# Performance work log

Measured on AMD Instinct MI355X. Metric: run time of the kernel, lower is better.

Reference implementation:

```python
import jax, jax.numpy as jnp
import numpy as np

D_IN = 1024
D_OUT = 1024
NUM_HEADS = 16
HEAD_DIM = D_OUT // NUM_HEADS


def setup_inputs() -> dict:
    key = jax.random.key(0)
    k_x, k_q, k_k, k_v, k_o = jax.random.split(key, 5)
    # Xavier-uniform-ish init for weights (stored as [d_in, d_out] for x @ W)
    lim = float(np.sqrt(6.0 / (D_IN + D_OUT)) / np.sqrt(2.0))
    lim_o = float(np.sqrt(6.0 / (D_OUT + D_OUT)))
    return {
        "x": jax.random.normal(k_x, (2, 2048, D_IN), dtype=jnp.float32),
        "W_query": jax.random.uniform(k_q, (D_IN, D_OUT), jnp.float32, -lim, lim),
        "W_key": jax.random.uniform(k_k, (D_IN, D_OUT), jnp.float32, -lim, lim),
        "W_value": jax.random.uniform(k_v, (D_IN, D_OUT), jnp.float32, -lim, lim),
        "W_out": jax.random.uniform(k_o, (D_OUT, D_OUT), jnp.float32, -lim_o, lim_o),
        "b_out": jnp.zeros((D_OUT,), dtype=jnp.float32),
    }


def reference(x, W_query, W_key, W_value, W_out, b_out):
    B, S, _ = x.shape
    scale = 1.0 / np.sqrt(HEAD_DIM)

    def split_heads(t):  # [B,S,D] -> [B,H,S,hd]
        return t.reshape(B, S, NUM_HEADS, HEAD_DIM).transpose(0, 2, 1, 3)

    q = split_heads(x @ W_query)
    k = split_heads(x @ W_key)
    v = split_heads(x @ W_value)

    scores = jnp.einsum("bhqd,bhkd->bhqk", q, k) * scale  # [B,H,S,S]
    causal = jnp.tril(jnp.ones((S, S), dtype=bool))  # True = keep
    scores = jnp.where(causal, scores, -jnp.inf)
    weights = jax.nn.softmax(scores, axis=-1)
    ctx = jnp.einsum("bhqk,bhkd->bhqd", weights, v)
    ctx = ctx.transpose(0, 2, 1, 3).reshape(B, S, D_OUT)
    return ctx @ W_out + b_out
```

## Files before the change

kernel.cpp:

```cpp
#include <hip/hip_runtime.h>
#include <hip/hip_bf16.h>


typedef __bf16 bf16_t;
typedef __bf16 bf16x4 __attribute__((ext_vector_type(4)));
typedef __bf16 bf16x8 __attribute__((ext_vector_type(8)));
typedef float f32x4 __attribute__((ext_vector_type(4)));

__device__ __forceinline__ void barrier_lgkm() {
    asm volatile("s_waitcnt lgkmcnt(0)\n\ts_barrier" ::: "memory");
}

__device__ __forceinline__ float exp_pwrite(f32x4 sc[4], bf16_t* Ps,
                                            int wave, int quad, int l16) {
    float part = 0.f;
    int rowbase = (wave * 16 + l16) * 64;
    int gran = (quad & 1) * 4;
    int chi = quad >> 1;
#pragma unroll
    for (int nt = 0; nt < 4; nt++) {
        f32x4 p;
#pragma unroll
        for (int rr = 0; rr < 4; rr++) {
            p[rr] = __builtin_amdgcn_exp2f(sc[nt][rr]);
            part += p[rr];
        }
        bf16x4 pb;
#pragma unroll
        for (int rr = 0; rr < 4; rr++) pb[rr] = (bf16_t)p[rr];
        int cc = (nt * 2 + chi) ^ (l16 & 7);
        *(bf16x4*)(Ps + rowbase + cc * 8 + gran) = pb;
    }
    part += __shfl_xor(part, 16);
    part += __shfl_xor(part, 32);
    return part;
}

__global__ __launch_bounds__(256) void prep_k(
    const float* __restrict__ x, const float* __restrict__ W0,
    const float* __restrict__ W1, const float* __restrict__ W2,
    const float* __restrict__ W3, bf16_t* __restrict__ xb,
    bf16_t* __restrict__ WTs) {
    __shared__ bf16_t T[64][65];
    int t = threadIdx.x;
    int blk = blockIdx.x;
    if (blk < 4096) {
        int i = blk * 256 + t;
        float4 v = ((const float4*)x)[i];
        bf16x4 o;
        o[0] = (bf16_t)v.x; o[1] = (bf16_t)v.y;
        o[2] = (bf16_t)v.z; o[3] = (bf16_t)v.w;
        ((bf16x4*)xb)[i] = o;
        return;
    }
    int jj = blk - 4096;
    int k0 = (jj & 15) * 64, n0 = ((jj >> 4) & 15) * 64, z = jj >> 8;
    const float* W = (z == 0) ? W0 : (z == 1) ? W1 : (z == 2) ? W2 : W3;
    bf16_t* WT = WTs + (size_t)z * 1048576;
#pragma unroll
    for (int c = 0; c < 4; c++) {
        int idx = c * 256 + t;
        int row = idx >> 4, col4 = (idx & 15) * 4;
        float4 v = *(const float4*)(W + (k0 + row) * 1024 + n0 + col4);
        T[row][col4 + 0] = (bf16_t)v.x;
        T[row][col4 + 1] = (bf16_t)v.y;
        T[row][col4 + 2] = (bf16_t)v.z;
        T[row][col4 + 3] = (bf16_t)v.w;
    }
    __syncthreads();
#pragma unroll
    for (int c = 0; c < 4; c++) {
        int idx = c * 256 + t;
        int nrow = idx >> 4, kc4 = (idx & 15) * 4;
        bf16x4 o;
        o[0] = T[kc4 + 0][nrow];
        o[1] = T[kc4 + 1][nrow];
        o[2] = T[kc4 + 2][nrow];
        o[3] = T[kc4 + 3][nrow];
        *(bf16x4*)(WT + (n0 + nrow) * 1024 + k0 + kc4) = o;
    }
}

__global__ __launch_bounds__(256) void qkv_k(
    const bf16_t* __restrict__ xb, const bf16_t* __restrict__ WTs,
    bf16_t* __restrict__ Qb, bf16_t* __restrict__ Kb, bf16_t* __restrict__ Vb) {
    const int KD = 1024;
    __shared__ __align__(16) bf16_t As[2][4096];
    __shared__ __align__(16) bf16_t Bs[2][4096];
    int tid = threadIdx.x;
    int wave = tid >> 6, lane = tid & 63;
    int quad = lane >> 4, l16 = lane & 15;
    int wm = wave >> 1, wn = wave & 1;
    int z = blockIdx.z;
    const bf16_t* BT = WTs + (size_t)z * 1048576;
    int m0 = blockIdx.x * 128;
    int n0 = blockIdx.y * 128;

    int r = tid >> 2;
    int c8 = (((tid & 3) ^ ((tid >> 3) & 3))) * 8;
    const bf16_t* gA0 = xb + (size_t)(m0 + r) * KD + c8;
    const bf16_t* gA1 = xb + (size_t)(m0 + 64 + r) * KD + c8;
    const bf16_t* gB0 = BT + (size_t)(n0 + r) * KD + c8;
    const bf16_t* gB1 = BT + (size_t)(n0 + 64 + r) * KD + c8;

    f32x4 acc[4][4];
#pragma unroll
    for (int i = 0; i < 4; i++)
#pragma unroll
        for (int j = 0; j < 4; j++) acc[i][j] = (f32x4){0.f, 0.f, 0.f, 0.f};

    int4 sa0 = *(const int4*)gA0, sa1 = *(const int4*)gA1;
    int4 sb0 = *(const int4*)gB0, sb1 = *(const int4*)gB1;
    *(int4*)(As[0] + tid * 8) = sa0;
    *(int4*)(As[0] + 2048 + tid * 8) = sa1;
    *(int4*)(Bs[0] + tid * 8) = sb0;
    *(int4*)(Bs[0] + 2048 + tid * 8) = sb1;
    sa0 = *(const int4*)(gA0 + 32); sa1 = *(const int4*)(gA1 + 32);
    sb0 = *(const int4*)(gB0 + 32); sb1 = *(const int4*)(gB1 + 32);

    int csw = (quad ^ ((l16 >> 1) & 3)) * 8;
#pragma unroll 1
    for (int kk = 0; kk < 32; kk += 2) {
        barrier_lgkm();
        bf16x8 af[4], bfr[4];
#pragma unroll
        for (int mt = 0; mt < 4; mt++)
            af[mt] = *(const bf16x8*)(As[0] + (wm * 64 + mt * 16 + l16) * 32 + csw);
#pragma unroll
        for (int nt = 0; nt < 4; nt++)
            bfr[nt] = *(const bf16x8*)(Bs[0] + (wn * 64 + nt * 16 + l16) * 32 + csw);
        *(int4*)(As[1] + tid * 8) = sa0;
        *(int4*)(As[1] + 2048 + tid * 8) = sa1;
        *(int4*)(Bs[1] + tid * 8) = sb0;
        *(int4*)(Bs[1] + 2048 + tid * 8) = sb1;
        if (kk + 2 < 32) {
            int k0 = (kk + 2) * 32;
            sa0 = *(const int4*)(gA0 + k0); sa1 = *(const int4*)(gA1 + k0);
            sb0 = *(const int4*)(gB0 + k0); sb1 = *(const int4*)(gB1 + k0);
        }
        if (z == 2) {
#pragma unroll
            for (int mt = 0; mt < 4; mt++)
#pragma unroll
                for (int nt = 0; nt < 4; nt++)
                    acc[mt][nt] = __builtin_amdgcn_mfma_f32_16x16x32_bf16(
                        bfr[nt], af[mt], acc[mt][nt], 0, 0, 0);
        } else {
#pragma unroll
            for (int mt = 0; mt < 4; mt++)
#pragma unroll
                for (int nt = 0; nt < 4; nt++)
                    acc[mt][nt] = __builtin_amdgcn_mfma_f32_16x16x32_bf16(
                        af[mt], bfr[nt], acc[mt][nt], 0, 0, 0);
        }
        barrier_lgkm();
#pragma unroll
        for (int mt = 0; mt < 4; mt++)
            af[mt] = *(const bf16x8*)(As[1] + (wm * 64 + mt * 16 + l16) * 32 + csw);
#pragma unroll
        for (int nt = 0; nt < 4; nt++)
            bfr[nt] = *(const bf16x8*)(Bs[1] + (wn * 64 + nt * 16 + l16) * 32 + csw);
        if (kk + 2 < 32) {
            *(int4*)(As[0] + tid * 8) = sa0;
            *(int4*)(As[0] + 2048 + tid * 8) = sa1;
            *(int4*)(Bs[0] + tid * 8) = sb0;
            *(int4*)(Bs[0] + 2048 + tid * 8) = sb1;
            if (kk + 3 < 32) {
                int k0 = (kk + 3) * 32;
                sa0 = *(const int4*)(gA0 + k0); sa1 = *(const int4*)(gA1 + k0);
                sb0 = *(const int4*)(gB0 + k0); sb1 = *(const int4*)(gB1 + k0);
            }
        }
        if (z == 2) {
#pragma unroll
            for (int mt = 0; mt < 4; mt++)
#pragma unroll
                for (int nt = 0; nt < 4; nt++)
                    acc[mt][nt] = __builtin_amdgcn_mfma_f32_16x16x32_bf16(
                        bfr[nt], af[mt], acc[mt][nt], 0, 0, 0);
        } else {
#pragma unroll
            for (int mt = 0; mt < 4; mt++)
#pragma unroll
                for (int nt = 0; nt < 4; nt++)
                    acc[mt][nt] = __builtin_amdgcn_mfma_f32_16x16x32_bf16(
                        af[mt], bfr[nt], acc[mt][nt], 0, 0, 0);
        }
    }

    if (z == 0) {
#pragma unroll
        for (int mt = 0; mt < 4; mt++) {
            int mg_base = m0 + wm * 64 + mt * 16 + quad * 4;
#pragma unroll
            for (int nt = 0; nt < 4; nt++) {
                int ng = n0 + wn * 64 + nt * 16 + l16;
                int h = ng >> 6, d = ng & 63;
#pragma unroll
                for (int rr = 0; rr < 4; rr++) {
                    int mg = mg_base + rr;
                    int b = mg >> 11, s = mg & 2047;
                    Qb[(((size_t)(b * 16 + h) * 2048) + s) * 64 + d] =
                        (bf16_t)acc[mt][nt][rr];
                }
            }
        }
    } else if (z == 1) {
#pragma unroll
        for (int mt = 0; mt < 4; mt++) {
            int mg_base = m0 + wm * 64 + mt * 16 + quad * 4;
#pragma unroll
            for (int nt = 0; nt < 4; nt++) {
                int ng = n0 + wn * 64 + nt * 16 + l16;
                int h = ng >> 6, dd = ng & 63;
#pragma unroll
                for (int rr = 0; rr < 4; rr++) {
                    int mg = mg_base + rr;
                    int b = mg >> 11, sl = mg & 2047;
                    int kt = sl >> 6, row = sl & 63;
                    int cc = (dd >> 3) ^ (row & 7);
                    Kb[(size_t)(b * 16 + h) * 131072 + kt * 4096 + row * 64 +
                       cc * 8 + (dd & 7)] = (bf16_t)acc[mt][nt][rr];
                }
            }
        }
    } else {
#pragma unroll
        for (int mt = 0; mt < 4; mt++) {
            int sg = m0 + wm * 64 + mt * 16 + l16;
            int b = sg >> 11, sl = sg & 2047;
            int kt = sl >> 6, srow = sl & 63;
#pragma unroll
            for (int nt = 0; nt < 4; nt++) {
                int dg_base = n0 + wn * 64 + nt * 16 + quad * 4;
#pragma unroll
                for (int rr = 0; rr < 4; rr++) {
                    int dg = dg_base + rr;
                    int h = dg >> 6, dd = dg & 63;
                    int cc = (srow >> 3) ^ (dd & 7);
                    Vb[(size_t)(b * 16 + h) * 131072 + kt * 4096 + dd * 64 +
                       cc * 8 + (srow & 7)] = (bf16_t)acc[mt][nt][rr];
                }
            }
        }
    }
}

__global__ __launch_bounds__(256) void attn_k(
    const bf16_t* __restrict__ Qb, const bf16_t* __restrict__ Kb,
    const bf16_t* __restrict__ Vb, bf16_t* __restrict__ ctxb) {
    const int S = 2048;
    __shared__ __align__(16) bf16_t Ps[2][4096];
    int tid = threadIdx.x, wave = tid >> 6, lane = tid & 63;
    int quad = lane >> 4, l16 = lane & 15;

    int f = blockIdx.x;
    int xcd = f & 7;
    int j = f >> 3;
    int hi = j >> 5;
    int idx = j & 31;
    int qtj = hi ? (15 - (idx & 15)) : (idx & 15);
    int bh = xcd * 4 + ((idx >> 4) + 2 * hi);
    int h = bh & 15, b = bh >> 4;
    int q0 = qtj * 128;

    const bf16_t* Qbh = Qb + (size_t)bh * S * 64;
    const bf16_t* Kbh = Kb + (size_t)bh * 131072;
    const bf16_t* Vbh = Vb + (size_t)bh * 131072;

    const float qs = 0.125f * 1.44269504f;
    bf16x8 aQ[2][2];
#pragma unroll
    for (int sub = 0; sub < 2; sub++) {
        const bf16_t* rq = Qbh + (size_t)(q0 + sub * 64 + wave * 16 + l16) * 64;
#pragma unroll
        for (int ks = 0; ks < 2; ks++) {
            bf16x8 t = *(const bf16x8*)(rq + ks * 32 + quad * 8);
#pragma unroll
            for (int jj = 0; jj < 8; jj++) t[jj] = (bf16_t)((float)t[jj] * qs);
            aQ[sub][ks] = t;
        }
    }

    float L[2] = {0.f, 0.f};
    f32x4 O[2][4];
#pragma unroll
    for (int sub = 0; sub < 2; sub++)
#pragma unroll
        for (int i = 0; i < 4; i++) O[sub][i] = (f32x4){0.f, 0.f, 0.f, 0.f};

    int koff[4][2];
#pragma unroll
    for (int nt = 0; nt < 4; nt++)
#pragma unroll
        for (int ks = 0; ks < 2; ks++)
            koff[nt][ks] = (nt * 16 + l16) * 64 + ((ks * 4 + quad) ^ (l16 & 7)) * 8;

    int tmax = 2 * qtj + 2;
#pragma unroll 1
    for (int kt = 0; kt < tmax; kt++) {
        const bf16_t* kbase = Kbh + kt * 4096;
        const bf16_t* vbase = Vbh + kt * 4096;
        bf16x8 kf[4][2], vf[4][2];
#pragma unroll
        for (int nt = 0; nt < 4; nt++)
#pragma unroll
            for (int ks = 0; ks < 2; ks++) {
                kf[nt][ks] = *(const bf16x8*)(kbase + koff[nt][ks]);
                vf[nt][ks] = *(const bf16x8*)(vbase + koff[nt][ks]);
            }

        bool do_lo = (kt < tmax - 1);
        if (do_lo) {
            f32x4 sc[4];
#pragma unroll
            for (int nt = 0; nt < 4; nt++) {
                f32x4 ss = (f32x4){0.f, 0.f, 0.f, 0.f};
                ss = __builtin_amdgcn_mfma_f32_16x16x32_bf16(kf[nt][0], aQ[0][0], ss, 0, 0, 0);
                ss = __builtin_amdgcn_mfma_f32_16x16x32_bf16(kf[nt][1], aQ[0][1], ss, 0, 0, 0);
                sc[nt] = ss;
            }
            if (kt == tmax - 2) {
                int qg = q0 + wave * 16 + l16;
#pragma unroll
                for (int nt = 0; nt < 4; nt++)
#pragma unroll
                    for (int rr = 0; rr < 4; rr++)
                        if (kt * 64 + nt * 16 + quad * 4 + rr > qg) sc[nt][rr] = -1e30f;
            }
            L[0] += exp_pwrite(sc, Ps[0], wave, quad, l16);
        }
        {
            f32x4 sc[4];
#pragma unroll
            for (int nt = 0; nt < 4; nt++) {
                f32x4 ss = (f32x4){0.f, 0.f, 0.f, 0.f};
                ss = __builtin_amdgcn_mfma_f32_16x16x32_bf16(kf[nt][0], aQ[1][0], ss, 0, 0, 0);
                ss = __builtin_amdgcn_mfma_f32_16x16x32_bf16(kf[nt][1], aQ[1][1], ss, 0, 0, 0);
                sc[nt] = ss;
            }
            if (kt == tmax - 1) {
                int qg = q0 + 64 + wave * 16 + l16;
#pragma unroll
                for (int nt = 0; nt < 4; nt++)
#pragma unroll
                    for (int rr = 0; rr < 4; rr++)
                        if (kt * 64 + nt * 16 + quad * 4 + rr > qg) sc[nt][rr] = -1e30f;
            }
            L[1] += exp_pwrite(sc, Ps[1], wave, quad, l16);
        }

#pragma unroll
        for (int ks = 0; ks < 2; ks++) {
            int csw = ((ks * 4 + quad) ^ (l16 & 7)) * 8;
            bf16x8 aPhi = *(const bf16x8*)(Ps[1] + (wave * 16 + l16) * 64 + csw);
            bf16x8 aPlo;
            if (do_lo) aPlo = *(const bf16x8*)(Ps[0] + (wave * 16 + l16) * 64 + csw);
#pragma unroll
            for (int nt = 0; nt < 4; nt++) {
                O[1][nt] = __builtin_amdgcn_mfma_f32_16x16x32_bf16(aPhi, vf[nt][ks],
                                                                   O[1][nt], 0, 0, 0);
                if (do_lo)
                    O[0][nt] = __builtin_amdgcn_mfma_f32_16x16x32_bf16(aPlo, vf[nt][ks],
                                                                       O[0][nt], 0, 0, 0);
            }
        }
    }

#pragma unroll
    for (int sub = 0; sub < 2; sub++) {
        float il[4];
#pragma unroll
        for (int rr = 0; rr < 4; rr++) il[rr] = 1.f / __shfl(L[sub], quad * 4 + rr);
#pragma unroll
        for (int nt = 0; nt < 4; nt++) {
#pragma unroll
            for (int rr = 0; rr < 4; rr++) {
                int qoff = q0 + sub * 64 + wave * 16 + quad * 4 + rr;
                int col = h * 64 + nt * 16 + l16;
                ctxb[(size_t)(b * 2048 + qoff) * 1024 + col] =
                    (bf16_t)(O[sub][nt][rr] * il[rr]);
            }
        }
    }
}

__global__ __launch_bounds__(256) void out_k(
    const bf16_t* __restrict__ ctxb, const bf16_t* __restrict__ WoT,
    const float* __restrict__ bo, float* __restrict__ out) {
    const int KD = 1024;
    __shared__ __align__(16) bf16_t As[2][2048];
    __shared__ __align__(16) bf16_t Bs[2][4096];
    int tid = threadIdx.x;
    int wave = tid >> 6, lane = tid & 63;
    int quad = lane >> 4, l16 = lane & 15;
    int wm = wave >> 1, wn = wave & 1;
    int m0 = blockIdx.x * 64;
    int n0 = blockIdx.y * 128;

    int r = tid >> 2;
    int c8 = (((tid & 3) ^ ((tid >> 3) & 3))) * 8;
    const bf16_t* gA  = ctxb + (size_t)(m0 + r) * KD + c8;
    const bf16_t* gB0 = WoT + (size_t)(n0 + r) * KD + c8;
    const bf16_t* gB1 = WoT + (size_t)(n0 + 64 + r) * KD + c8;

    f32x4 acc[2][4];
#pragma unroll
    for (int i = 0; i < 2; i++)
#pragma unroll
        for (int j = 0; j < 4; j++) acc[i][j] = (f32x4){0.f, 0.f, 0.f, 0.f};

    int4 sa = *(const int4*)gA;
    int4 sb0 = *(const int4*)gB0, sb1 = *(const int4*)gB1;
    *(int4*)(As[0] + tid * 8) = sa;
    *(int4*)(Bs[0] + tid * 8) = sb0;
    *(int4*)(Bs[0] + 2048 + tid * 8) = sb1;
    sa = *(const int4*)(gA + 32);
    sb0 = *(const int4*)(gB0 + 32); sb1 = *(const int4*)(gB1 + 32);

    int csw = (quad ^ ((l16 >> 1) & 3)) * 8;
#pragma unroll 1
    for (int kk = 0; kk < 32; kk += 2) {
        barrier_lgkm();
        bf16x8 af[2], bfr[4];
#pragma unroll
        for (int mt = 0; mt < 2; mt++)
            af[mt] = *(const bf16x8*)(As[0] + (wm * 32 + mt * 16 + l16) * 32 + csw);
#pragma unroll
        for (int nt = 0; nt < 4; nt++)
            bfr[nt] = *(const bf16x8*)(Bs[0] + (wn * 64 + nt * 16 + l16) * 32 + csw);
        *(int4*)(As[1] + tid * 8) = sa;
        *(int4*)(Bs[1] + tid * 8) = sb0;
        *(int4*)(Bs[1] + 2048 + tid * 8) = sb1;
        if (kk + 2 < 32) {
            int k0 = (kk + 2) * 32;
            sa = *(const int4*)(gA + k0);
            sb0 = *(const int4*)(gB0 + k0); sb1 = *(const int4*)(gB1 + k0);
        }
#pragma unroll
        for (int mt = 0; mt < 2; mt++)
#pragma unroll
            for (int nt = 0; nt < 4; nt++)
                acc[mt][nt] = __builtin_amdgcn_mfma_f32_16x16x32_bf16(
                    af[mt], bfr[nt], acc[mt][nt], 0, 0, 0);
        barrier_lgkm();
#pragma unroll
        for (int mt = 0; mt < 2; mt++)
            af[mt] = *(const bf16x8*)(As[1] + (wm * 32 + mt * 16 + l16) * 32 + csw);
#pragma unroll
        for (int nt = 0; nt < 4; nt++)
            bfr[nt] = *(const bf16x8*)(Bs[1] + (wn * 64 + nt * 16 + l16) * 32 + csw);
        if (kk + 2 < 32) {
            *(int4*)(As[0] + tid * 8) = sa;
            *(int4*)(Bs[0] + tid * 8) = sb0;
            *(int4*)(Bs[0] + 2048 + tid * 8) = sb1;
            if (kk + 3 < 32) {
                int k0 = (kk + 3) * 32;
                sa = *(const int4*)(gA + k0);
                sb0 = *(const int4*)(gB0 + k0); sb1 = *(const int4*)(gB1 + k0);
            }
        }
#pragma unroll
        for (int mt = 0; mt < 2; mt++)
#pragma unroll
            for (int nt = 0; nt < 4; nt++)
                acc[mt][nt] = __builtin_amdgcn_mfma_f32_16x16x32_bf16(
                    af[mt], bfr[nt], acc[mt][nt], 0, 0, 0);
    }

#pragma unroll
    for (int mt = 0; mt < 2; mt++) {
        int mg_base = m0 + wm * 32 + mt * 16 + quad * 4;
#pragma unroll
        for (int nt = 0; nt < 4; nt++) {
            int ng = n0 + wn * 64 + nt * 16 + l16;
            float bv = bo[ng];
#pragma unroll
            for (int rr = 0; rr < 4; rr++) {
                int mg = mg_base + rr;
                out[(size_t)mg * 1024 + ng] = acc[mt][nt][rr] + bv;
            }
        }
    }
}

extern "C" void kernel_launch(void* const* d_in, const int* in_sizes, int n_in,
                              void* d_out, int out_size, void* d_ws, size_t ws_size,
                              hipStream_t stream) {
    const float* x  = (const float*)d_in[0];
    const float* Wq = (const float*)d_in[1];
    const float* Wk = (const float*)d_in[2];
    const float* Wv = (const float*)d_in[3];
    const float* Wo = (const float*)d_in[4];
    const float* bo = (const float*)d_in[5];
    float* out = (float*)d_out;
    char* ws = (char*)d_ws;

    bf16_t* xb   = (bf16_t*)ws;
    bf16_t* WTs  = (bf16_t*)(ws + (8u << 20));
    bf16_t* Qb   = (bf16_t*)(ws + (16u << 20));
    bf16_t* Kb   = (bf16_t*)(ws + (24u << 20));
    bf16_t* Vb   = (bf16_t*)(ws + (32u << 20));
    bf16_t* ctxb = (bf16_t*)(ws + (40u << 20));

    prep_k<<<5120, 256, 0, stream>>>(x, Wq, Wk, Wv, Wo, xb, WTs);
    qkv_k<<<dim3(32, 8, 3), 256, 0, stream>>>(xb, WTs, Qb, Kb, Vb);
    attn_k<<<512, 256, 0, stream>>>(Qb, Kb, Vb, ctxb);
    out_k<<<dim3(64, 8), 256, 0, stream>>>(ctxb, WTs + 3145728, bo, out);
}
```

Baseline: 177.7 us.

## Use persistent atomic work queue for causal attention with 64-row query tiles

```diff
diff --git a/kernel.cpp b/kernel.cpp
--- a/kernel.cpp
+++ b/kernel.cpp
@@ -6,6 +6,8 @@
 typedef __bf16 bf16x4 __attribute__((ext_vector_type(4)));
 typedef __bf16 bf16x8 __attribute__((ext_vector_type(8)));
 typedef float f32x4 __attribute__((ext_vector_type(4)));
+
+__device__ int g_job;
 
 __device__ __forceinline__ void barrier_lgkm() {
     asm volatile("s_waitcnt lgkmcnt(0)\n\ts_barrier" ::: "memory");
@@ -44,6 +46,7 @@
     __shared__ bf16_t T[64][65];
     int t = threadIdx.x;
     int blk = blockIdx.x;
+    if (blk == 0 && t == 0) g_job = 0;
     if (blk < 4096) {
         int i = blk * 256 + t;
         float4 v = ((const float4*)x)[i];
@@ -250,44 +253,11 @@
     const bf16_t* __restrict__ Qb, const bf16_t* __restrict__ Kb,
     const bf16_t* __restrict__ Vb, bf16_t* __restrict__ ctxb) {
     const int S = 2048;
-    __shared__ __align__(16) bf16_t Ps[2][4096];
+    __shared__ __align__(16) bf16_t Ps[4096];
+    __shared__ int s_job;
     int tid = threadIdx.x, wave = tid >> 6, lane = tid & 63;
     int quad = lane >> 4, l16 = lane & 15;
-
-    int f = blockIdx.x;
-    int xcd = f & 7;
-    int j = f >> 3;
-    int hi = j >> 5;
-    int idx = j & 31;
-    int qtj = hi ? (15 - (idx & 15)) : (idx & 15);
-    int bh = xcd * 4 + ((idx >> 4) + 2 * hi);
-    int h = bh & 15, b = bh >> 4;
-    int q0 = qtj * 128;
-
-    const bf16_t* Qbh = Qb + (size_t)bh * S * 64;
-    const bf16_t* Kbh = Kb + (size_t)bh * 131072;
-    const bf16_t* Vbh = Vb + (size_t)bh * 131072;
-
     const float qs = 0.125f * 1.44269504f;
-    bf16x8 aQ[2][2];
-#pragma unroll
-    for (int sub = 0; sub < 2; sub++) {
-        const bf16_t* rq = Qbh + (size_t)(q0 + sub * 64 + wave * 16 + l16) * 64;
-#pragma unroll
-        for (int ks = 0; ks < 2; ks++) {
-            bf16x8 t = *(const bf16x8*)(rq + ks * 32 + quad * 8);
-#pragma unroll
-            for (int jj = 0; jj < 8; jj++) t[jj] = (bf16_t)((float)t[jj] * qs);
-            aQ[sub][ks] = t;
-        }
-    }
-
-    float L[2] = {0.f, 0.f};
-    f32x4 O[2][4];
-#pragma unroll
-    for (int sub = 0; sub < 2; sub++)
-#pragma unroll
-        for (int i = 0; i < 4; i++) O[sub][i] = (f32x4){0.f, 0.f, 0.f, 0.f};
 
     int koff[4][2];
 #pragma unroll
@@ -296,31 +266,61 @@
         for (int ks = 0; ks < 2; ks++)
             koff[nt][ks] = (nt * 16 + l16) * 64 + ((ks * 4 + quad) ^ (l16 & 7)) * 8;
 
-    int tmax = 2 * qtj + 2;
 #pragma unroll 1
-    for (int kt = 0; kt < tmax; kt++) {
-        const bf16_t* kbase = Kbh + kt * 4096;
-        const bf16_t* vbase = Vbh + kt * 4096;
-        bf16x8 kf[4][2], vf[4][2];
-#pragma unroll
-        for (int nt = 0; nt < 4; nt++)
+    while (true) {
+        __syncthreads();
+        if (tid == 0) s_job = atomicAdd(&g_job, 1);
+        __syncthreads();
+        int j = s_job;
+        if (j >= 1024) break;
+        int qt = 31 - (j >> 5);
+        int bh = j & 31;
+        int h = bh & 15, b = bh >> 4;
+        int q0 = qt * 64;
+
+        const bf16_t* Qbh = Qb + (size_t)bh * S * 64;
+        const bf16_t* Kbh = Kb + (size_t)bh * 131072;
+        const bf16_t* Vbh = Vb + (size_t)bh * 131072;
+
+        bf16x8 aQ[2];
+        {
+            const bf16_t* rq = Qbh + (size_t)(q0 + wave * 16 + l16) * 64;
 #pragma unroll
             for (int ks = 0; ks < 2; ks++) {
-                kf[nt][ks] = *(const bf16x8*)(kbase + koff[nt][ks]);
-                vf[nt][ks] = *(const bf16x8*)(vbase + koff[nt][ks]);
-            }
-
-        bool do_lo = (kt < tmax - 1);
-        if (do_lo) {
+                bf16x8 t = *(const bf16x8*)(rq + ks * 32 + quad * 8);
+#pragma unroll
+                for (int jj = 0; jj < 8; jj++) t[jj] = (bf16_t)((float)t[jj] * qs);
+                aQ[ks] = t;
+            }
+        }
+
+        float L = 0.f;
+        f32x4 O[4];
+#pragma unroll
+        for (int i = 0; i < 4; i++) O[i] = (f32x4){0.f, 0.f, 0.f, 0.f};
+
+#pragma unroll 1
+        for (int kt = 0; kt <= qt; kt++) {
+            const bf16_t* kbase = Kbh + kt * 4096;
+            const bf16_t* vbase = Vbh + kt * 4096;
+            bf16x8 kf[4][2], vf[4][2];
+#pragma unroll
+            for (int nt = 0; nt < 4; nt++)
+#pragma unroll
+                for (int ks = 0; ks < 2; ks++) {
+                    kf[nt][ks] = *(const bf16x8*)(kbase + koff[nt][ks]);
+                    vf[nt][ks] = *(const bf16x8*)(vbase + koff[nt][ks]);
+                }
+
             f32x4 sc[4];
 #pragma unroll
             for (int nt = 0; nt < 4; nt++) {
                 f32x4 ss = (f32x4){0.f, 0.f, 0.f, 0.f};
-                ss = __builtin_amdgcn_mfma_f32_16x16x32_bf16(kf[nt][0], aQ[0][0], ss, 0, 0, 0);
-                ss = __builtin_amdgcn_mfma_f32_16x16x32_bf16(kf[nt][1], aQ[0][1], ss, 0, 0, 0);
+                ss = __builtin_amdgcn_mfma_f32_16x16x32_bf16(kf[nt][0], aQ[0], ss, 0, 0, 0);
+                ss = __builtin_amdgcn_mfma_f32_16x16x32_bf16(kf[nt][1], aQ[1], ss, 0, 0, 0);
                 sc[nt] = ss;
             }
-            if (kt == tmax - 2) {
+            if (kt == qt) {
                 int qg = q0 + wave * 16 + l16;
 #pragma unroll
                 for (int nt = 0; nt < 4; nt++)
@@ -328,58 +328,30 @@
                     for (int rr = 0; rr < 4; rr++)
                         if (kt * 64 + nt * 16 + quad * 4 + rr > qg) sc[nt][rr] = -1e30f;
             }
-            L[0] += exp_pwrite(sc, Ps[0], wave, quad, l16);
-        }
-        {
-            f32x4 sc[4];
-#pragma unroll
-            for (int nt = 0; nt < 4; nt++) {
-                f32x4 ss = (f32x4){0.f, 0.f, 0.f, 0.f};
-                ss = __builtin_amdgcn_mfma_f32_16x16x32_bf16(kf[nt][0], aQ[1][0], ss, 0, 0, 0);
-                ss = __builtin_amdgcn_mfma_f32_16x16x32_bf16(kf[nt][1], aQ[1][1], ss, 0, 0, 0);
-                sc[nt] = ss;
-            }
-            if (kt == tmax - 1) {
-                int qg = q0 + 64 + wave * 16 + l16;
-#pragma unroll
-                for (int nt = 0; nt < 4; nt++)
-#pragma unroll
-                    for (int rr = 0; rr < 4; rr++)
-                        if (kt * 64 + nt * 16 + quad * 4 + rr > qg) sc[nt][rr] = -1e30f;
-            }
-            L[1] += exp_pwrite(sc, Ps[1], wave, quad, l16);
-        }
-
-#pragma unroll
-        for (int ks = 0; ks < 2; ks++) {
-            int csw = ((ks * 4 + quad) ^ (l16 & 7)) * 8;
-            bf16x8 aPhi = *(const bf16x8*)(Ps[1] + (wave * 16 + l16) * 64 + csw);
-            bf16x8 aPlo;
-            if (do_lo) aPlo = *(const bf16x8*)(Ps[0] + (wave * 16 + l16) * 64 + csw);
-#pragma unroll
-            for (int nt = 0; nt < 4; nt++) {
-                O[1][nt] = __builtin_amdgcn_mfma_f32_16x16x32_bf16(aPhi, vf[nt][ks],
-                                                                   O[1][nt], 0, 0, 0);
-                if (do_lo)
-                    O[0][nt] = __builtin_amdgcn_mfma_f32_16x16x32_bf16(aPlo, vf[nt][ks],
-                                                                       O[0][nt], 0, 0, 0);
-            }
-        }
-    }
-
-#pragma unroll
-    for (int sub = 0; sub < 2; sub++) {
+            L += exp_pwrite(sc, Ps, wave, quad, l16);
+
+#pragma unroll
+            for (int ks = 0; ks < 2; ks++) {
+                int csw = ((ks * 4 + quad) ^ (l16 & 7)) * 8;
+                bf16x8 aP = *(const bf16x8*)(Ps + (wave * 16 + l16) * 64 + csw);
+#pragma unroll
+                for (int nt = 0; nt < 4; nt++)
+                    O[nt] = __builtin_amdgcn_mfma_f32_16x16x32_bf16(aP, vf[nt][ks],
+                                                                    O[nt], 0, 0, 0);
+            }
+        }
+
         float il[4];
 #pragma unroll
-        for (int rr = 0; rr < 4; rr++) il[rr] = 1.f / __shfl(L[sub], quad * 4 + rr);
+        for (int rr = 0; rr < 4; rr++) il[rr] = 1.f / __shfl(L, quad * 4 + rr);
 #pragma unroll
         for (int nt = 0; nt < 4; nt++) {
 #pragma unroll
             for (int rr = 0; rr < 4; rr++) {
-                int qoff = q0 + sub * 64 + wave * 16 + quad * 4 + rr;
+                int qoff = q0 + wave * 16 + quad * 4 + rr;
                 int col = h * 64 + nt * 16 + l16;
                 ctxb[(size_t)(b * 2048 + qoff) * 1024 + col] =
-                    (bf16_t)(O[sub][nt][rr] * il[rr]);
+                    (bf16_t)(O[nt][rr] * il[rr]);
             }
         }
     }
```

Result: slower. 197.0 us (+10.9%).

## Split attention into single-wave workgroups with longest-first causal scheduling

Applied to the files above, without the earlier changes.

```diff
diff --git a/kernel.cpp b/kernel.cpp
--- a/kernel.cpp
+++ b/kernel.cpp
@@ -12,9 +12,9 @@
 }
 
 __device__ __forceinline__ float exp_pwrite(f32x4 sc[4], bf16_t* Ps,
-                                            int wave, int quad, int l16) {
+                                            int quad, int l16) {
     float part = 0.f;
-    int rowbase = (wave * 16 + l16) * 64;
+    int rowbase = l16 * 64;
     int gran = (quad & 1) * 4;
     int chi = quad >> 1;
 #pragma unroll
@@ -246,21 +246,21 @@
     }
 }
 
-__global__ __launch_bounds__(256) void attn_k(
+__global__ __launch_bounds__(64) void attn_k(
     const bf16_t* __restrict__ Qb, const bf16_t* __restrict__ Kb,
     const bf16_t* __restrict__ Vb, bf16_t* __restrict__ ctxb) {
     const int S = 2048;
-    __shared__ __align__(16) bf16_t Ps[2][4096];
-    int tid = threadIdx.x, wave = tid >> 6, lane = tid & 63;
+    __shared__ __align__(16) bf16_t Ps[2][1024];
+    int lane = threadIdx.x & 63;
     int quad = lane >> 4, l16 = lane & 15;
 
     int f = blockIdx.x;
     int xcd = f & 7;
-    int j = f >> 3;
-    int hi = j >> 5;
-    int idx = j & 31;
-    int qtj = hi ? (15 - (idx & 15)) : (idx & 15);
-    int bh = xcd * 4 + ((idx >> 4) + 2 * hi);
+    int r = f >> 3;
+    int qtj = 15 - (r >> 4);
+    int rl = r & 15;
+    int bh = xcd * 4 + (rl >> 2);
+    int wgrp = rl & 3;
     int h = bh & 15, b = bh >> 4;
     int q0 = qtj * 128;
 
@@ -272,7 +272,7 @@
     bf16x8 aQ[2][2];
 #pragma unroll
     for (int sub = 0; sub < 2; sub++) {
-        const bf16_t* rq = Qbh + (size_t)(q0 + sub * 64 + wave * 16 + l16) * 64;
+        const bf16_t* rq = Qbh + (size_t)(q0 + sub * 64 + wgrp * 16 + l16) * 64;
 #pragma unroll
         for (int ks = 0; ks < 2; ks++) {
             bf16x8 t = *(const bf16x8*)(rq + ks * 32 + quad * 8);
@@ -321,14 +321,14 @@
                 sc[nt] = ss;
             }
             if (kt == tmax - 2) {
-                int qg = q0 + wave * 16 + l16;
+                int qg = q0 + wgrp * 16 + l16;
 #pragma unroll
                 for (int nt = 0; nt < 4; nt++)
 #pragma unroll
                     for (int rr = 0; rr < 4; rr++)
                         if (kt * 64 + nt * 16 + quad * 4 + rr > qg) sc[nt][rr] = -1e30f;
             }
-            L[0] += exp_pwrite(sc, Ps[0], wave, quad, l16);
+            L[0] += exp_pwrite(sc, Ps[0], quad, l16);
         }
         {
             f32x4 sc[4];
@@ -340,22 +340,22 @@
                 sc[nt] = ss;
             }
             if (kt == tmax - 1) {
-                int qg = q0 + 64 + wave * 16 + l16;
+                int qg = q0 + 64 + wgrp * 16 + l16;
 #pragma unroll
                 for (int nt = 0; nt < 4; nt++)
 #pragma unroll
                     for (int rr = 0; rr < 4; rr++)
                         if (kt * 64 + nt * 16 + quad * 4 + rr > qg) sc[nt][rr] = -1e30f;
             }
-            L[1] += exp_pwrite(sc, Ps[1], wave, quad, l16);
+            L[1] += exp_pwrite(sc, Ps[1], quad, l16);
         }
 
 #pragma unroll
         for (int ks = 0; ks < 2; ks++) {
             int csw = ((ks * 4 + quad) ^ (l16 & 7)) * 8;
-            bf16x8 aPhi = *(const bf16x8*)(Ps[1] + (wave * 16 + l16) * 64 + csw);
+            bf16x8 aPhi = *(const bf16x8*)(Ps[1] + l16 * 64 + csw);
             bf16x8 aPlo;
-            if (do_lo) aPlo = *(const bf16x8*)(Ps[0] + (wave * 16 + l16) * 64 + csw);
+            if (do_lo) aPlo = *(const bf16x8*)(Ps[0] + l16 * 64 + csw);
 #pragma unroll
             for (int nt = 0; nt < 4; nt++) {
                 O[1][nt] = __builtin_amdgcn_mfma_f32_16x16x32_bf16(aPhi, vf[nt][ks],
@@ -376,7 +376,7 @@
         for (int nt = 0; nt < 4; nt++) {
 #pragma unroll
             for (int rr = 0; rr < 4; rr++) {
-                int qoff = q0 + sub * 64 + wave * 16 + quad * 4 + rr;
+                int qoff = q0 + sub * 64 + wgrp * 16 + quad * 4 + rr;
                 int col = h * 64 + nt * 16 + l16;
                 ctxb[(size_t)(b * 2048 + qoff) * 1024 + col] =
                     (bf16_t)(O[sub][nt][rr] * il[rr]);
@@ -505,6 +505,6 @@
 
     prep_k<<<5120, 256, 0, stream>>>(x, Wq, Wk, Wv, Wo, xb, WTs);
     qkv_k<<<dim3(32, 8, 3), 256, 0, stream>>>(xb, WTs, Qb, Kb, Vb);
-    attn_k<<<512, 256, 0, stream>>>(Qb, Kb, Vb, ctxb);
+    attn_k<<<2048, 64, 0, stream>>>(Qb, Kb, Vb, ctxb);
     out_k<<<dim3(64, 8), 256, 0, stream>>>(ctxb, WTs + 3145728, bo, out);
 }
```

Result: no change. 176.0 us, median of 2 (-0.9%).
